# Performance work log

Hardware: AMD Instinct MI355X
Metric: run time of the kernel (lower is better)

## Reference

```python
import jax, jax.numpy as jnp
import numpy as np

OUT = 7                # adaptive pool output size (7,7)
SPATIAL_SCALE = 1.0 / 16.0
NEG = jnp.float32(-3.0e38)  # acts as -inf for masked max


def setup_inputs() -> dict:
    key = jax.random.key(0)
    k1, k2, k3, k4, k5, k6 = jax.random.split(key, 6)
    B, C, H, W = 2, 256, 50, 50
    R = 256
    features = jax.random.normal(k1, (B, C, H, W), dtype=jnp.float32)
    # boxes in image coordinates (image = 800x800, stride 16)
    x1 = jax.random.uniform(k2, (R,), minval=0.0, maxval=500.0)
    y1 = jax.random.uniform(k3, (R,), minval=0.0, maxval=500.0)
    bw = jax.random.uniform(k4, (R,), minval=64.0, maxval=296.0)
    bh = jax.random.uniform(k5, (R,), minval=64.0, maxval=296.0)
    rois = jnp.stack([x1, y1, x1 + bw, y1 + bh], axis=1).astype(jnp.float32)  # [R,4]
    roi_indices = jax.random.randint(k6, (R,), 0, B, dtype=jnp.int64)
    return {"features": features, "rois": rois, "roi_indices": roi_indices}


def _roi_pool(features, rois, roi_indices):
    H, W = features.shape[2], features.shape[3]
    ri = (rois * SPATIAL_SCALE).astype(jnp.int32)           # truncation, as np.astype
    x1, y1, x2, y2 = ri[:, 0], ri[:, 1], ri[:, 2], ri[:, 3]
    # NOTE: original code slices features[idx, :, x1:x2, y1:y2] -> x indexes dim H, y indexes dim W
    Lh = x2 - x1                                            # [R]
    Lw = y2 - y1
    p = jnp.arange(OUT)
    # adaptive max pool bin boundaries (torch semantics): start=floor(i*L/OUT), end=ceil((i+1)*L/OUT)
    hstart = x1[:, None] + (p[None, :] * Lh[:, None]) // OUT                   # [R,OUT]
    hend = x1[:, None] + ((p[None, :] + 1) * Lh[:, None] + OUT - 1) // OUT
    wstart = y1[:, None] + (p[None, :] * Lw[:, None]) // OUT
    wend = y1[:, None] + ((p[None, :] + 1) * Lw[:, None] + OUT - 1) // OUT
    hidx = jnp.arange(H)
    widx = jnp.arange(W)
    row_mask = (hidx[None, None, :] >= hstart[:, :, None]) & (hidx[None, None, :] < hend[:, :, None])  # [R,OUT,H]
    col_mask = (widx[None, None, :] >= wstart[:, :, None]) & (widx[None, None, :] < wend[:, :, None])  # [R,OUT,W]

    feat = features[roi_indices]                            # [R,C,H,W]
    # reduce over W per output column (fixed small loop over OUT bins)
    cols = []
    for pw in range(OUT):
        m = col_mask[:, pw][:, None, None, :]               # [R,1,1,W]
        cols.append(jnp.max(jnp.where(m, feat, NEG), axis=3))  # [R,C,H]
    t = jnp.stack(cols, axis=-1)                            # [R,C,H,OUT]
    # reduce over H per output row
    rows = []
    for ph in range(OUT):
        m = row_mask[:, ph][:, None, :, None]               # [R,1,H,1]
        rows.append(jnp.max(jnp.where(m, t, NEG), axis=2))  # [R,C,OUT]
    return jnp.stack(rows, axis=2)                          # [R,C,OUT,OUT]


def reference(features, rois, roi_indices):
    return _roi_pool(features, rois, roi_indices)
```

## Files before the change

kernel.cpp:

```cpp
#include <hip/hip_runtime.h>
#include <cstddef>
#include <cstdint>


namespace {
constexpr int OUTP = 7;
constexpr int BB = 2;
constexpr int CC = 256;
constexpr int HH = 50;
constexpr int WW = 50;
constexpr int HWSZ = HH * WW;
constexpr float NEGV = -3e38f;
}

__global__ __launch_bounds__(256) void transpose_k(const float* __restrict__ in,
                                                   float* __restrict__ out) {
    __shared__ float tile[32][33];
    const int b = blockIdx.z;
    const int hw0 = blockIdx.x * 32;
    const int c0 = blockIdx.y * 32;
    const int tx = threadIdx.x;
#pragma unroll
    for (int i = threadIdx.y; i < 32; i += 8) {
        const int hw = hw0 + tx;
        float v = 0.0f;
        if (hw < HWSZ) v = in[(size_t)(b * CC + c0 + i) * HWSZ + hw];
        tile[i][tx] = v;
    }
    __syncthreads();
#pragma unroll
    for (int i = threadIdx.y; i < 32; i += 8) {
        const int hw = hw0 + i;
        if (hw < HWSZ) out[(size_t)(b * HWSZ + hw) * CC + c0 + tx] = tile[tx][i];
    }
}

__global__ __launch_bounds__(256) void roipool_fast(const float* __restrict__ feat,
                                                    const float* __restrict__ rois,
                                                    const int* __restrict__ ridx,
                                                    float* __restrict__ out) {
    const int r = blockIdx.x;
    const int ph = blockIdx.y;
    const int c = threadIdx.x;

    const float4 rv = reinterpret_cast<const float4*>(rois)[r];
    int x1 = (int)(rv.x * 0.0625f);
    int y1 = (int)(rv.y * 0.0625f);
    int x2 = (int)(rv.z * 0.0625f);
    int y2 = (int)(rv.w * 0.0625f);
    int b = ridx[r];
    x1 = __builtin_amdgcn_readfirstlane(x1);
    y1 = __builtin_amdgcn_readfirstlane(y1);
    x2 = __builtin_amdgcn_readfirstlane(x2);
    y2 = __builtin_amdgcn_readfirstlane(y2);
    b = __builtin_amdgcn_readfirstlane(b);

    const int Lh = x2 - x1;
    const int Lw = y2 - y1;

    int hs = x1 + (ph * Lh) / OUTP;
    int he = x1 + ((ph + 1) * Lh + OUTP - 1) / OUTP;
    hs = hs < 0 ? 0 : hs;
    he = he > HH ? HH : he;
    const int nh = he - hs;

    int ws_[OUTP], nw_[OUTP];
    int mx = nh;
#pragma unroll
    for (int p = 0; p < OUTP; ++p) {
        int a = y1 + (p * Lw) / OUTP;
        int e = y1 + ((p + 1) * Lw + OUTP - 1) / OUTP;
        a = a < 0 ? 0 : a;
        e = e > WW ? WW : e;
        ws_[p] = a;
        nw_[p] = e - a;
        mx = mx > (e - a) ? mx : (e - a);
    }

    float acc[OUTP];
#pragma unroll
    for (int p = 0; p < OUTP; ++p) acc[p] = NEGV;

    const float* base = feat + ((size_t)(b * HH + hs) * WW) * CC + c;

    if (mx <= 4) {
#pragma unroll
        for (int hh = 0; hh < 4; ++hh) {
            if (hh < nh) {
                const float* rp = base + (size_t)hh * (WW * CC);
#pragma unroll
                for (int p = 0; p < OUTP; ++p) {
#pragma unroll
                    for (int ww = 0; ww < 4; ++ww) {
                        int col = ws_[p] + ww;
                        col = col > (WW - 1) ? (WW - 1) : col;
                        const float v = rp[(size_t)col * CC];
                        const float vv = (ww < nw_[p]) ? v : NEGV;
                        acc[p] = fmaxf(acc[p], vv);
                    }
                }
            }
        }
    } else {
        for (int hh = 0; hh < nh; ++hh) {
            const float* rp = base + (size_t)hh * (WW * CC);
#pragma unroll
            for (int p = 0; p < OUTP; ++p) {
                for (int ww = 0; ww < nw_[p]; ++ww) {
                    acc[p] = fmaxf(acc[p], rp[(size_t)(ws_[p] + ww) * CC]);
                }
            }
        }
    }

    float* op = out + ((size_t)r * CC + c) * (OUTP * OUTP) + (size_t)ph * OUTP;
#pragma unroll
    for (int p = 0; p < OUTP; ++p) op[p] = acc[p];
}

__global__ __launch_bounds__(256) void roipool_generic(const float* __restrict__ feat,
                                                       const float* __restrict__ rois,
                                                       const int* __restrict__ ridx,
                                                       float* __restrict__ out) {
    const int r = blockIdx.x;
    const int ph = blockIdx.y;
    const int c = threadIdx.x;

    const float4 rv = reinterpret_cast<const float4*>(rois)[r];
    const int x1 = (int)(rv.x * 0.0625f);
    const int y1 = (int)(rv.y * 0.0625f);
    const int x2 = (int)(rv.z * 0.0625f);
    const int y2 = (int)(rv.w * 0.0625f);
    const int b = ridx[r];
    const int Lh = x2 - x1;
    const int Lw = y2 - y1;

    int hs = x1 + (ph * Lh) / OUTP;
    int he = x1 + ((ph + 1) * Lh + OUTP - 1) / OUTP;
    hs = hs < 0 ? 0 : hs;
    he = he > HH ? HH : he;

    float acc[OUTP];
#pragma unroll
    for (int p = 0; p < OUTP; ++p) acc[p] = NEGV;

    for (int h = hs; h < he; ++h) {
#pragma unroll
        for (int p = 0; p < OUTP; ++p) {
            int w0 = y1 + (p * Lw) / OUTP;
            int w1 = y1 + ((p + 1) * Lw + OUTP - 1) / OUTP;
            w0 = w0 < 0 ? 0 : w0;
            w1 = w1 > WW ? WW : w1;
            float m = acc[p];
            for (int w = w0; w < w1; ++w) {
                m = fmaxf(m, feat[((size_t)(b * CC + c) * HH + h) * WW + w]);
            }
            acc[p] = m;
        }
    }

    float* op = out + ((size_t)r * CC + c) * (OUTP * OUTP) + (size_t)ph * OUTP;
#pragma unroll
    for (int p = 0; p < OUTP; ++p) op[p] = acc[p];
}

extern "C" void kernel_launch(void* const* d_in, const int* in_sizes, int n_in,
                              void* d_out, int out_size, void* d_ws, size_t ws_size,
                              hipStream_t stream) {
    const float* features = (const float*)d_in[0];
    const float* rois = (const float*)d_in[1];
    const int* ridx = (const int*)d_in[2];
    float* out = (float*)d_out;
    const int R = in_sizes[1] / 4;

    const size_t tbytes = (size_t)BB * HWSZ * CC * sizeof(float);
    if (ws_size >= tbytes) {
        float* featT = (float*)d_ws;
        dim3 tg((HWSZ + 31) / 32, CC / 32, BB);
        transpose_k<<<tg, dim3(32, 8), 0, stream>>>(features, featT);
        roipool_fast<<<dim3(R, OUTP), 256, 0, stream>>>(featT, rois, ridx, out);
    } else {
        roipool_generic<<<dim3(R, OUTP), 256, 0, stream>>>(features, rois, ridx, out);
    }
}
```

Measured before the change: 24.18 us.

## Split channels into groups, fuse all output rows per block, stage output via LDS

The transpose now writes features as [split][B][HW][64] so each channel quarter is contiguous. The pool kernel uses one block per (channel group, ROI) with 448 threads covering all 7 output rows. Results are staged in shared memory and written out as coalesced nontemporal stores instead of strided 7-float writes per thread. This targets uncoalesced output writes and improves locality of the gathered feature reads, at the cost of extra LDS and a block-wide sync.

```diff
diff --git a/kernel.cpp b/kernel.cpp
--- a/kernel.cpp
+++ b/kernel.cpp
@@ -10,6 +10,8 @@
 constexpr int HH = 50;
 constexpr int WW = 50;
 constexpr int HWSZ = HH * WW;
+constexpr int CSPLIT = 4;
+constexpr int CPS = CC / CSPLIT;
 constexpr float NEGV = -3e38f;
 }
 
@@ -28,20 +30,26 @@
         tile[i][tx] = v;
     }
     __syncthreads();
+    const int ch = c0 + tx;
+    const int s = ch >> 6;
+    const int cin = ch & 63;
 #pragma unroll
     for (int i = threadIdx.y; i < 32; i += 8) {
         const int hw = hw0 + i;
-        if (hw < HWSZ) out[(size_t)(b * HWSZ + hw) * CC + c0 + tx] = tile[tx][i];
-    }
-}
-
-__global__ __launch_bounds__(256) void roipool_fast(const float* __restrict__ feat,
-                                                    const float* __restrict__ rois,
-                                                    const int* __restrict__ ridx,
-                                                    float* __restrict__ out) {
-    const int r = blockIdx.x;
-    const int ph = blockIdx.y;
-    const int c = threadIdx.x;
+        if (hw < HWSZ)
+            out[((size_t)((s * BB + b) * HWSZ) + hw) * CPS + cin] = tile[tx][i];
+    }
+}
+
+__global__ __launch_bounds__(448) void roipool3(const float* __restrict__ feat,
+                                                const float* __restrict__ rois,
+                                                const int* __restrict__ ridx,
+                                                float* __restrict__ out) {
+    const int s = blockIdx.x;
+    const int r = blockIdx.y;
+    const int tid = threadIdx.x;
+    const int c = tid & 63;
+    const int ph = __builtin_amdgcn_readfirstlane(tid >> 6);
 
     const float4 rv = reinterpret_cast<const float4*>(rois)[r];
     int x1 = (int)(rv.x * 0.0625f);
@@ -81,20 +89,20 @@
 #pragma unroll
     for (int p = 0; p < OUTP; ++p) acc[p] = NEGV;
 
-    const float* base = feat + ((size_t)(b * HH + hs) * WW) * CC + c;
+    const float* base = feat + ((size_t)((s * BB + b) * HWSZ) + (size_t)hs * WW) * CPS + c;
 
     if (mx <= 4) {
 #pragma unroll
         for (int hh = 0; hh < 4; ++hh) {
             if (hh < nh) {
-                const float* rp = base + (size_t)hh * (WW * CC);
+                const float* rp = base + (size_t)hh * (WW * CPS);
 #pragma unroll
                 for (int p = 0; p < OUTP; ++p) {
 #pragma unroll
                     for (int ww = 0; ww < 4; ++ww) {
                         int col = ws_[p] + ww;
                         col = col > (WW - 1) ? (WW - 1) : col;
-                        const float v = rp[(size_t)col * CC];
+                        const float v = rp[(size_t)col * CPS];
                         const float vv = (ww < nw_[p]) ? v : NEGV;
                         acc[p] = fmaxf(acc[p], vv);
                     }
@@ -103,19 +111,26 @@
         }
     } else {
         for (int hh = 0; hh < nh; ++hh) {
-            const float* rp = base + (size_t)hh * (WW * CC);
+            const float* rp = base + (size_t)hh * (WW * CPS);
 #pragma unroll
             for (int p = 0; p < OUTP; ++p) {
                 for (int ww = 0; ww < nw_[p]; ++ww) {
-                    acc[p] = fmaxf(acc[p], rp[(size_t)(ws_[p] + ww) * CC]);
+                    acc[p] = fmaxf(acc[p], rp[(size_t)(ws_[p] + ww) * CPS]);
                 }
             }
         }
     }
 
-    float* op = out + ((size_t)r * CC + c) * (OUTP * OUTP) + (size_t)ph * OUTP;
-#pragma unroll
-    for (int p = 0; p < OUTP; ++p) op[p] = acc[p];
+    __shared__ float st[CPS * OUTP * OUTP];
+#pragma unroll
+    for (int p = 0; p < OUTP; ++p) st[c * 49 + ph * OUTP + p] = acc[p];
+    __syncthreads();
+
+    float* ob = out + ((size_t)(r * CC + s * CPS)) * (OUTP * OUTP);
+#pragma unroll
+    for (int k = 0; k < OUTP; ++k) {
+        __builtin_nontemporal_store(st[tid + k * 448], ob + tid + k * 448);
+    }
 }
 
 __global__ __launch_bounds__(256) void roipool_generic(const float* __restrict__ feat,
@@ -174,11 +189,11 @@
     const int R = in_sizes[1] / 4;
 
     const size_t tbytes = (size_t)BB * HWSZ * CC * sizeof(float);
-    if (ws_size >= tbytes) {
+    if (ws_size >= tbytes && (R % 1) == 0) {
         float* featT = (float*)d_ws;
         dim3 tg((HWSZ + 31) / 32, CC / 32, BB);
         transpose_k<<<tg, dim3(32, 8), 0, stream>>>(features, featT);
-        roipool_fast<<<dim3(R, OUTP), 256, 0, stream>>>(featT, rois, ridx, out);
+        roipool3<<<dim3(CSPLIT, R), 448, 0, stream>>>(featT, rois, ridx, out);
     } else {
         roipool_generic<<<dim3(R, OUTP), 256, 0, stream>>>(features, rois, ridx, out);
     }
```

Result: faster. 21.12 us (-12.6%).
